# Kernel tuning notes

Measured on AMD Instinct MI355X. Metric: run time of the kernel, lower is better.

Reference implementation:

```python
import jax, jax.numpy as jnp
import numpy as np

DIM = 512
NUM_HEADS = 8
HEAD_DIM = DIM // NUM_HEADS
MAX_SIZE = 128


def setup_inputs() -> dict:
    key = jax.random.key(0)
    ks = jax.random.split(key, 13)
    B, C, H, W = 4, DIM, 128, 128
    inp = {
        "x": jax.random.normal(ks[0], (B, C, H, W), jnp.float32),
        "q_w": jax.random.normal(ks[1], (DIM, DIM), jnp.float32) * 0.02,
        "q_b": jax.random.normal(ks[2], (DIM,), jnp.float32) * 0.02,
        "k_w": jax.random.normal(ks[3], (DIM, DIM), jnp.float32) * 0.02,
        "k_b": jax.random.normal(ks[4], (DIM,), jnp.float32) * 0.02,
        "v_w": jax.random.normal(ks[5], (DIM, DIM), jnp.float32) * 0.02,
        "v_b": jax.random.normal(ks[6], (DIM,), jnp.float32) * 0.02,
        "o_w": jax.random.normal(ks[7], (DIM, DIM), jnp.float32) * 0.02,
        "o_b": jax.random.normal(ks[8], (DIM,), jnp.float32) * 0.02,
        "pos_q": jax.random.normal(ks[9], (1, NUM_HEADS, MAX_SIZE, HEAD_DIM), jnp.float32),
        "pos_k": jax.random.normal(ks[10], (1, NUM_HEADS, MAX_SIZE, HEAD_DIM), jnp.float32),
        "pos_v": jax.random.normal(ks[11], (1, NUM_HEADS, MAX_SIZE, HEAD_DIM), jnp.float32),
        "g_q": jnp.ones((1,), jnp.float32),
        "g_k": jnp.ones((1,), jnp.float32),
        "g_v1": jnp.ones((1,), jnp.float32),
        "g_v2": jnp.ones((1,), jnp.float32),
    }
    return inp


def _gated_axial_attn(x, q_w, q_b, k_w, k_b, v_w, v_b, o_w, o_b,
                      pos_q, pos_k, pos_v, g_q, g_k, g_v1, g_v2):
    B, C, H, W = x.shape
    nh, hd = NUM_HEADS, C // NUM_HEADS
    scale = hd ** (-0.5)
    # axis='width': attend along W for each (B,H) row
    xf = jnp.transpose(x, (0, 2, 3, 1)).reshape(B * H, W, C)  # (BH, W, C)

    def proj(w, b):
        y = xf @ w.T + b                       # (BH, W, C)
        return jnp.transpose(y.reshape(B * H, W, nh, hd), (0, 2, 1, 3))  # (BH, nh, W, hd)

    q = proj(q_w, q_b)
    k = proj(k_w, k_b)
    v = proj(v_w, v_b)

    pq = pos_q[0, :, :W, :]  # (nh, W, hd)
    pk = pos_k[0, :, :W, :]
    pv = pos_v[0, :, :W, :]

    # scores[i,j] = q_i.k_j + g_q * q_i.pq_j + g_k * pk_i.k_j, all scaled
    scores = jnp.einsum('bnid,bnjd->bnij', q, k)
    scores = scores + g_q[0] * jnp.einsum('bnid,njd->bnij', q, pq)
    scores = scores + g_k[0] * jnp.einsum('nid,bnjd->bnij', pk, k)
    attn = jax.nn.softmax(scores * scale, axis=-1)  # (BH, nh, W, W)

    vmix = g_v1[0] * v + g_v2[0] * pv[None]        # (BH, nh, W, hd)
    out = jnp.einsum('bnij,bnjd->bnid', attn, vmix)
    out = jnp.transpose(out, (0, 2, 1, 3)).reshape(B * H, W, C)
    out = out @ o_w.T + o_b
    return jnp.transpose(out.reshape(B, H, W, C), (0, 3, 1, 2))  # (B, C, H, W)


def reference(x, q_w, q_b, k_w, k_b, v_w, v_b, o_w, o_b,
              pos_q, pos_k, pos_v, g_q, g_k, g_v1, g_v2):
    return _gated_axial_attn(x, q_w, q_b, k_w, k_b, v_w, v_b, o_w, o_b,
                             pos_q, pos_k, pos_v, g_q, g_k, g_v1, g_v2)
```

## Files before the change

kernel.cpp:

```cpp
#include <hip/hip_runtime.h>

typedef __bf16 bf16;
typedef __attribute__((ext_vector_type(8))) __bf16 bf16x8;
typedef __attribute__((ext_vector_type(4))) __bf16 bf16x4;
typedef __attribute__((ext_vector_type(4))) float fvec4;

#define MFMA16(a, b, c) __builtin_amdgcn_mfma_f32_16x16x32_bf16(a, b, c, 0, 0, 0)

__device__ __forceinline__ void glds16(const bf16* g, bf16* l) {
  __builtin_amdgcn_global_load_lds(
      (const __attribute__((address_space(1))) void*)g,
      (__attribute__((address_space(3))) void*)l, 16, 0, 0);
}

__device__ inline fvec4 zero4() { fvec4 z = {0.f, 0.f, 0.f, 0.f}; return z; }

#define PREP_ELEMS 1245184

__global__ __launch_bounds__(512) void prep_kernel(
    const float* __restrict__ qw, const float* __restrict__ kw,
    const float* __restrict__ vw, const float* __restrict__ ow,
    const float* __restrict__ pq, const float* __restrict__ pk,
    const float* __restrict__ pv, bf16* __restrict__ dst)
{
  int i = (blockIdx.x * 512 + threadIdx.x) * 4;
  const float* s;
  if      (i < 262144)  s = qw + i;
  else if (i < 524288)  s = kw + (i - 262144);
  else if (i < 786432)  s = vw + (i - 524288);
  else if (i < 1048576) s = ow + (i - 786432);
  else if (i < 1114112) s = pq + (i - 1048576);
  else if (i < 1179648) s = pk + (i - 1114112);
  else                  s = pv + (i - 1179648);
  fvec4 v = *(const fvec4*)s;
  bf16x4 o = { (bf16)v[0], (bf16)v[1], (bf16)v[2], (bf16)v[3] };
  *(bf16x4*)(dst + i) = o;
}

__global__ __launch_bounds__(256) void xpose_kernel(
    const float* __restrict__ x, bf16* __restrict__ xt, int bh0)
{
  __shared__ float Xs[64 * 133];
  const int cb = blockIdx.x, lb = blockIdx.y;
  const int bh = bh0 + lb, b = bh >> 7, h = bh & 127;
  const int t = threadIdx.x;
  const float* xb = x + (size_t)b * 8388608 + (size_t)(cb * 64) * 16384 + h * 128;
  #pragma unroll
  for (int it = 0; it < 8; ++it) {
    int idx = it * 256 + t;
    int c = idx >> 5, w4 = (idx & 31) << 2;
    fvec4 v = *(const fvec4*)(xb + (size_t)c * 16384 + w4);
    #pragma unroll
    for (int j = 0; j < 4; ++j) Xs[c * 133 + w4 + j] = v[j];
  }
  __syncthreads();
  const int c0 = (t & 7) * 8, wsub = t >> 3;
  #pragma unroll
  for (int wb = 0; wb < 4; ++wb) {
    int w = wb * 32 + wsub;
    bf16x8 o;
    #pragma unroll
    for (int i = 0; i < 8; ++i) o[i] = (bf16)Xs[(c0 + i) * 133 + w];
    *(bf16x8*)(xt + ((size_t)lb * 128 + w) * 512 + cb * 64 + c0) = o;
  }
}

__global__ __launch_bounds__(512, 4) void qkvattn_kernel(
    const bf16* __restrict__ xt, const bf16* __restrict__ wqkv,
    const float* __restrict__ q_b, const float* __restrict__ k_b,
    const float* __restrict__ v_b, const bf16* __restrict__ posb,
    const float* __restrict__ g_q, const float* __restrict__ g_k,
    const float* __restrict__ g_v1, const float* __restrict__ g_v2,
    bf16* __restrict__ ao)
{
  __shared__ bf16 SM[26624];
  bf16* As = SM;
  bf16* Bs = SM + 8192;
  bf16* Qs = SM;
  bf16* KP = SM + 9216;
  bf16* Vt = SM;

  const int nwg = gridDim.x;
  int wg = blockIdx.x;
  wg = (wg & 7) * (nwg >> 3) + (wg >> 3);
  const int lb = wg >> 3, n = wg & 7;

  const int t = threadIdx.x;
  const int wv = t >> 6, lane = t & 63;
  const int lr = lane & 15, lg = lane >> 4;
  const int srow = lane >> 3, c16 = lane & 7;

  fvec4 acc[12];
  #pragma unroll
  for (int i = 0; i < 12; ++i) acc[i] = zero4();

  const bf16* asrc[2];
  const bf16* bsrc[3];
  #pragma unroll
  for (int j = 0; j < 2; ++j) {
    int seg = wv * 2 + j;
    int row = seg * 8 + srow;
    int cs = c16 ^ (row & 7);
    asrc[j] = xt + (size_t)(lb * 128 + row) * 512 + cs * 8;
  }
  #pragma unroll
  for (int j = 0; j < 3; ++j) {
    int seg = wv * 3 + j;
    int row = seg * 8 + srow;
    int grow = ((row >> 6) << 9) + (n << 6) + (row & 63);
    int cs = c16 ^ (row & 7);
    bsrc[j] = wqkv + (size_t)grow * 512 + cs * 8;
  }

  for (int k0 = 0; k0 < 512; k0 += 64) {
    __syncthreads();
    #pragma unroll
    for (int j = 0; j < 2; ++j)
      glds16(asrc[j] + k0, As + (wv * 2 + j) * 512);
    #pragma unroll
    for (int j = 0; j < 3; ++j)
      glds16(bsrc[j] + k0, Bs + (wv * 3 + j) * 512);
    __syncthreads();
    #pragma unroll
    for (int kc = 0; kc < 2; ++kc) {
      int arow = wv * 16 + lr;
      int acs = (kc * 4 + lg) ^ (arow & 7);
      bf16x8 af = *(const bf16x8*)(As + arow * 64 + acs * 8);
      #pragma unroll
      for (int nt = 0; nt < 12; ++nt) {
        int brow = nt * 16 + lr;
        int bcs = (kc * 4 + lg) ^ (brow & 7);
        bf16x8 bfv = *(const bf16x8*)(Bs + brow * 64 + bcs * 8);
        acc[nt] = MFMA16(af, bfv, acc[nt]);
      }
    }
  }
  __syncthreads();

  const float gq = g_q[0], gk = g_k[0], gv1 = g_v1[0], gv2 = g_v2[0];
  const bf16* pqb = posb + (size_t)n * 8192;
  const bf16* pkb = posb + 65536 + (size_t)n * 8192;
  const bf16* pvb = posb + 131072 + (size_t)n * 8192;
  const int i0 = wv * 16;

  #pragma unroll
  for (int nt = 0; nt < 4; ++nt) {
    float bq = q_b[n * 64 + nt * 16 + lr];
    #pragma unroll
    for (int r = 0; r < 4; ++r)
      Qs[(i0 + lg * 4 + r) * 72 + nt * 16 + lr] = (bf16)(acc[nt][r] + bq);
  }
  #pragma unroll
  for (int nt = 0; nt < 4; ++nt) {
    int d = nt * 16 + lr;
    float bk = k_b[n * 64 + d];
    #pragma unroll
    for (int r = 0; r < 4; ++r) {
      int jr = i0 + lg * 4 + r;
      float kv = acc[4 + nt][r] + bk;
      float pqv = (float)pqb[jr * 64 + d];
      KP[jr * 136 + d]      = (bf16)(kv + gq * pqv);
      KP[jr * 136 + 64 + d] = (bf16)kv;
    }
  }
  __syncthreads();

  fvec4 s[8];
  #pragma unroll
  for (int i = 0; i < 8; ++i) s[i] = zero4();
  #pragma unroll
  for (int kc = 0; kc < 4; ++kc) {
    bf16x8 af;
    if (kc < 2) {
      af = *(const bf16x8*)(Qs + (i0 + lr) * 72 + kc * 32 + lg * 8);
    } else {
      bf16x8 raw = *(const bf16x8*)(pkb + (i0 + lr) * 64 + (kc - 2) * 32 + lg * 8);
      #pragma unroll
      for (int i = 0; i < 8; ++i) af[i] = (bf16)(gk * (float)raw[i]);
    }
    #pragma unroll
    for (int jt = 0; jt < 8; ++jt) {
      bf16x8 bfr = *(const bf16x8*)(KP + (jt * 16 + lr) * 136 + kc * 32 + lg * 8);
      s[jt] = MFMA16(af, bfr, s[jt]);
    }
  }

  const float scale = 0.125f;
  float inv[4];
  #pragma unroll
  for (int r = 0; r < 4; ++r) {
    float m = -1e30f;
    #pragma unroll
    for (int jt = 0; jt < 8; ++jt) m = fmaxf(m, s[jt][r]);
    #pragma unroll
    for (int off = 1; off < 16; off <<= 1) m = fmaxf(m, __shfl_xor(m, off));
    float sm = 0.f;
    #pragma unroll
    for (int jt = 0; jt < 8; ++jt) {
      float e = __expf((s[jt][r] - m) * scale);
      s[jt][r] = e;
      sm += e;
    }
    #pragma unroll
    for (int off = 1; off < 16; off <<= 1) sm += __shfl_xor(sm, off);
    inv[r] = 1.f / sm;
  }
  __syncthreads();

  #pragma unroll
  for (int r = 0; r < 4; ++r) {
    int i = i0 + lg * 4 + r;
    #pragma unroll
    for (int jt = 0; jt < 8; ++jt)
      KP[i * 136 + jt * 16 + lr] = (bf16)(s[jt][r] * inv[r]);
  }
  #pragma unroll
  for (int nt = 0; nt < 4; ++nt) {
    int d = nt * 16 + lr;
    float bv = v_b[n * 64 + d];
    #pragma unroll
    for (int r = 0; r < 4; ++r) {
      int jr = i0 + lg * 4 + r;
      Vt[d * 136 + jr] =
          (bf16)(gv1 * (acc[8 + nt][r] + bv) + gv2 * (float)pvb[jr * 64 + d]);
    }
  }
  __syncthreads();

  fvec4 o[4];
  #pragma unroll
  for (int i = 0; i < 4; ++i) o[i] = zero4();
  #pragma unroll
  for (int kc = 0; kc < 4; ++kc) {
    bf16x8 af = *(const bf16x8*)(KP + (i0 + lr) * 136 + kc * 32 + lg * 8);
    #pragma unroll
    for (int dt = 0; dt < 4; ++dt) {
      bf16x8 bfr = *(const bf16x8*)(Vt + (dt * 16 + lr) * 136 + kc * 32 + lg * 8);
      o[dt] = MFMA16(af, bfr, o[dt]);
    }
  }
  #pragma unroll
  for (int dt = 0; dt < 4; ++dt) {
    #pragma unroll
    for (int r = 0; r < 4; ++r) {
      int i = i0 + lg * 4 + r;
      ao[((size_t)lb * 128 + i) * 512 + n * 64 + dt * 16 + lr] = (bf16)o[dt][r];
    }
  }
}

__global__ __launch_bounds__(256, 3) void oproj_kernel(
    const bf16* __restrict__ ao, const bf16* __restrict__ wo,
    const float* __restrict__ o_b, float* __restrict__ out, int bh0)
{
  __shared__ bf16 As[128 * 64];
  __shared__ bf16 Bs[128 * 64];
  const int nwg = gridDim.x;
  int wg = blockIdx.x;
  if ((nwg & 7) == 0) wg = (wg & 7) * (nwg >> 3) + (wg >> 3);
  const int ct4 = wg & 3;
  const int lb = wg >> 2;
  const int bh = bh0 + lb, b = bh >> 7, h = bh & 127;
  const int t = threadIdx.x;
  const int wv = t >> 6, lane = t & 63;
  const int lr = lane & 15, lg = lane >> 4;
  const int wm = wv >> 1, wn = wv & 1;
  const int srow = lane >> 3, c16 = lane & 7;

  fvec4 acc[4][4];
  #pragma unroll
  for (int i = 0; i < 4; ++i)
    #pragma unroll
    for (int j = 0; j < 4; ++j) acc[i][j] = zero4();

  for (int k0 = 0; k0 < 512; k0 += 64) {
    __syncthreads();
    #pragma unroll
    for (int j = 0; j < 4; ++j) {
      int seg = wv * 4 + j;
      int row = seg * 8 + srow;
      int cs = c16 ^ (row & 7);
      glds16(wo + (size_t)(ct4 * 128 + row) * 512 + k0 + cs * 8, As + seg * 512);
      glds16(ao + ((size_t)lb * 128 + row) * 512 + k0 + cs * 8, Bs + seg * 512);
    }
    __syncthreads();
    #pragma unroll
    for (int kc = 0; kc < 2; ++kc) {
      bf16x8 af[4], bfv[4];
      #pragma unroll
      for (int mt = 0; mt < 4; ++mt) {
        int row = wm * 64 + mt * 16 + lr;
        int cs = (kc * 4 + lg) ^ (row & 7);
        af[mt] = *(const bf16x8*)(As + row * 64 + cs * 8);
      }
      #pragma unroll
      for (int nt = 0; nt < 4; ++nt) {
        int row = wn * 64 + nt * 16 + lr;
        int cs = (kc * 4 + lg) ^ (row & 7);
        bfv[nt] = *(const bf16x8*)(Bs + row * 64 + cs * 8);
      }
      #pragma unroll
      for (int mt = 0; mt < 4; ++mt)
        #pragma unroll
        for (int nt = 0; nt < 4; ++nt)
          acc[mt][nt] = MFMA16(af[mt], bfv[nt], acc[mt][nt]);
    }
  }
  #pragma unroll
  for (int mt = 0; mt < 4; ++mt) {
    #pragma unroll
    for (int r = 0; r < 4; ++r) {
      int co = ct4 * 128 + wm * 64 + mt * 16 + lg * 4 + r;
      float bv = o_b[co];
      size_t ob = ((size_t)(b * 512 + co) * 128 + h) * 128;
      #pragma unroll
      for (int nt = 0; nt < 4; ++nt) {
        int w = wn * 64 + nt * 16 + lr;
        out[ob + w] = acc[mt][nt][r] + bv;
      }
    }
  }
}

extern "C" void kernel_launch(void* const* d_in, const int* in_sizes, int n_in,
                              void* d_out, int out_size, void* d_ws, size_t ws_size,
                              hipStream_t stream) {
  const float* x    = (const float*)d_in[0];
  const float* q_w  = (const float*)d_in[1];
  const float* q_b  = (const float*)d_in[2];
  const float* k_w  = (const float*)d_in[3];
  const float* k_b  = (const float*)d_in[4];
  const float* v_w  = (const float*)d_in[5];
  const float* v_b  = (const float*)d_in[6];
  const float* o_w  = (const float*)d_in[7];
  const float* o_b  = (const float*)d_in[8];
  const float* pos_q = (const float*)d_in[9];
  const float* pos_k = (const float*)d_in[10];
  const float* pos_v = (const float*)d_in[11];
  const float* g_q  = (const float*)d_in[12];
  const float* g_k  = (const float*)d_in[13];
  const float* g_v1 = (const float*)d_in[14];
  const float* g_v2 = (const float*)d_in[15];
  float* out = (float*)d_out;

  bf16* prep = (bf16*)d_ws;
  bf16* wqkv = prep;
  bf16* wo   = prep + 786432;
  bf16* posb = prep + 1048576;

  bf16* rest = prep + PREP_ELEMS;
  size_t avail = (ws_size > (size_t)PREP_ELEMS * 2) ? ws_size - (size_t)PREP_ELEMS * 2 : 0;
  const size_t per_bh = (size_t)(65536 + 65536) * sizeof(bf16);
  int nbh = (int)(avail / per_bh);
  if (nbh > 512) nbh = 512;
  if (nbh < 1) nbh = 1;

  bf16* xt = rest;
  bf16* ao = xt + (size_t)nbh * 65536;

  prep_kernel<<<608, 512, 0, stream>>>(q_w, k_w, v_w, o_w, pos_q, pos_k, pos_v, prep);

  for (int bh0 = 0; bh0 < 512; bh0 += nbh) {
    int cur = (512 - bh0 < nbh) ? (512 - bh0) : nbh;
    xpose_kernel<<<dim3(8, cur), 256, 0, stream>>>(x, xt, bh0);
    qkvattn_kernel<<<cur * 8, 512, 0, stream>>>(xt, wqkv, q_b, k_b, v_b, posb,
                                                g_q, g_k, g_v1, g_v2, ao);
    oproj_kernel<<<cur * 4, 256, 0, stream>>>(ao, wo, o_b, out, bh0);
  }
}
```

Before: 510.5 us.

## Double-buffer QKV GEMM loads and retile warps to 2x6 MFMA blocks

The QKV projection loop in the fused attention kernel now double-buffers its LDS tiles, prefetching the next K-slice with global_load_lds while MFMAs run on the current one, which removes one barrier per iteration. The 8 waves are rearranged into a 4x2 grid, each computing 2x6 MFMA tiles instead of 1x12, so loaded fragments are reused more. The padded LDS layouts for Q, K/P and V^T are replaced with XOR-swizzled unpadded layouts. In exchange, shared memory grows from about 52KB to 80KB per block, which may lower occupancy below the requested 4 blocks per CU, and the epilogue gains section branching.

```diff
diff --git a/kernel.cpp b/kernel.cpp
--- a/kernel.cpp
+++ b/kernel.cpp
@@ -73,11 +73,9 @@
     const float* __restrict__ g_v1, const float* __restrict__ g_v2,
     bf16* __restrict__ ao)
 {
-  __shared__ bf16 SM[26624];
-  bf16* As = SM;
-  bf16* Bs = SM + 8192;
+  __shared__ bf16 SM[40960];
   bf16* Qs = SM;
-  bf16* KP = SM + 9216;
+  bf16* KP = SM + 8192;
   bf16* Vt = SM;
 
   const int nwg = gridDim.x;
@@ -89,10 +87,13 @@
   const int wv = t >> 6, lane = t & 63;
   const int lr = lane & 15, lg = lane >> 4;
   const int srow = lane >> 3, c16 = lane & 7;
-
-  fvec4 acc[12];
-  #pragma unroll
-  for (int i = 0; i < 12; ++i) acc[i] = zero4();
+  const int wm2 = wv >> 1, wn2 = wv & 1;
+
+  fvec4 acc[2][6];
+  #pragma unroll
+  for (int i = 0; i < 2; ++i)
+    #pragma unroll
+    for (int j = 0; j < 6; ++j) acc[i][j] = zero4();
 
   const bf16* asrc[2];
   const bf16* bsrc[3];
@@ -112,28 +113,46 @@
     bsrc[j] = wqkv + (size_t)grow * 512 + cs * 8;
   }
 
+  #pragma unroll
+  for (int j = 0; j < 2; ++j) glds16(asrc[j], SM + (wv * 2 + j) * 512);
+  #pragma unroll
+  for (int j = 0; j < 3; ++j) glds16(bsrc[j], SM + 8192 + (wv * 3 + j) * 512);
+
+  int cur = 0;
   for (int k0 = 0; k0 < 512; k0 += 64) {
     __syncthreads();
-    #pragma unroll
-    for (int j = 0; j < 2; ++j)
-      glds16(asrc[j] + k0, As + (wv * 2 + j) * 512);
-    #pragma unroll
-    for (int j = 0; j < 3; ++j)
-      glds16(bsrc[j] + k0, Bs + (wv * 3 + j) * 512);
-    __syncthreads();
+    if (k0 < 448) {
+      bf16* Ad = SM + (cur ^ 1) * 20480;
+      bf16* Bd = Ad + 8192;
+      #pragma unroll
+      for (int j = 0; j < 2; ++j) glds16(asrc[j] + k0 + 64, Ad + (wv * 2 + j) * 512);
+      #pragma unroll
+      for (int j = 0; j < 3; ++j) glds16(bsrc[j] + k0 + 64, Bd + (wv * 3 + j) * 512);
+    }
+    const bf16* Ab = SM + cur * 20480;
+    const bf16* Bb = Ab + 8192;
     #pragma unroll
     for (int kc = 0; kc < 2; ++kc) {
-      int arow = wv * 16 + lr;
-      int acs = (kc * 4 + lg) ^ (arow & 7);
-      bf16x8 af = *(const bf16x8*)(As + arow * 64 + acs * 8);
-      #pragma unroll
-      for (int nt = 0; nt < 12; ++nt) {
-        int brow = nt * 16 + lr;
-        int bcs = (kc * 4 + lg) ^ (brow & 7);
-        bf16x8 bfv = *(const bf16x8*)(Bs + brow * 64 + bcs * 8);
-        acc[nt] = MFMA16(af, bfv, acc[nt]);
-      }
-    }
+      bf16x8 af[2], bfv[6];
+      #pragma unroll
+      for (int mt = 0; mt < 2; ++mt) {
+        int row = wm2 * 32 + mt * 16 + lr;
+        int cs = (kc * 4 + lg) ^ (row & 7);
+        af[mt] = *(const bf16x8*)(Ab + row * 64 + cs * 8);
+      }
+      #pragma unroll
+      for (int nt = 0; nt < 6; ++nt) {
+        int row = wn2 * 96 + nt * 16 + lr;
+        int cs = (kc * 4 + lg) ^ (row & 7);
+        bfv[nt] = *(const bf16x8*)(Bb + row * 64 + cs * 8);
+      }
+      #pragma unroll
+      for (int mt = 0; mt < 2; ++mt)
+        #pragma unroll
+        for (int nt = 0; nt < 6; ++nt)
+          acc[mt][nt] = MFMA16(af[mt], bfv[nt], acc[mt][nt]);
+    }
+    cur ^= 1;
   }
   __syncthreads();
 
@@ -141,30 +160,41 @@
   const bf16* pqb = posb + (size_t)n * 8192;
   const bf16* pkb = posb + 65536 + (size_t)n * 8192;
   const bf16* pvb = posb + 131072 + (size_t)n * 8192;
+
+  #pragma unroll
+  for (int mt = 0; mt < 2; ++mt) {
+    #pragma unroll
+    for (int nt = 0; nt < 6; ++nt) {
+      int gc = wn2 * 96 + nt * 16 + lr;
+      int sec = gc >> 6;
+      int d = gc & 63;
+      int rb = wm2 * 32 + mt * 16 + lg * 4;
+      if (sec == 0) {
+        float bq = q_b[n * 64 + d];
+        #pragma unroll
+        for (int r = 0; r < 4; ++r) {
+          int row = rb + r;
+          Qs[row * 64 + (((d >> 3) ^ (row & 7)) << 3) + (d & 7)] =
+              (bf16)(acc[mt][nt][r] + bq);
+        }
+      } else if (sec == 1) {
+        float bk = k_b[n * 64 + d];
+        #pragma unroll
+        for (int r = 0; r < 4; ++r) {
+          int row = rb + r;
+          float kv = acc[mt][nt][r] + bk;
+          float pqv = (float)pqb[row * 64 + d];
+          KP[row * 128 + (((d >> 3) ^ (row & 7)) << 3) + (d & 7)] =
+              (bf16)(kv + gq * pqv);
+          int d2 = 64 + d;
+          KP[row * 128 + (((d2 >> 3) ^ (row & 7)) << 3) + (d2 & 7)] = (bf16)kv;
+        }
+      }
+    }
+  }
+  __syncthreads();
+
   const int i0 = wv * 16;
-
-  #pragma unroll
-  for (int nt = 0; nt < 4; ++nt) {
-    float bq = q_b[n * 64 + nt * 16 + lr];
-    #pragma unroll
-    for (int r = 0; r < 4; ++r)
-      Qs[(i0 + lg * 4 + r) * 72 + nt * 16 + lr] = (bf16)(acc[nt][r] + bq);
-  }
-  #pragma unroll
-  for (int nt = 0; nt < 4; ++nt) {
-    int d = nt * 16 + lr;
-    float bk = k_b[n * 64 + d];
-    #pragma unroll
-    for (int r = 0; r < 4; ++r) {
-      int jr = i0 + lg * 4 + r;
-      float kv = acc[4 + nt][r] + bk;
-      float pqv = (float)pqb[jr * 64 + d];
-      KP[jr * 136 + d]      = (bf16)(kv + gq * pqv);
-      KP[jr * 136 + 64 + d] = (bf16)kv;
-    }
-  }
-  __syncthreads();
-
   fvec4 s[8];
   #pragma unroll
   for (int i = 0; i < 8; ++i) s[i] = zero4();
@@ -172,7 +202,9 @@
   for (int kc = 0; kc < 4; ++kc) {
     bf16x8 af;
     if (kc < 2) {
-      af = *(const bf16x8*)(Qs + (i0 + lr) * 72 + kc * 32 + lg * 8);
+      int row = i0 + lr;
+      int cs = (kc * 4 + lg) ^ (row & 7);
+      af = *(const bf16x8*)(Qs + row * 64 + cs * 8);
     } else {
       bf16x8 raw = *(const bf16x8*)(pkb + (i0 + lr) * 64 + (kc - 2) * 32 + lg * 8);
       #pragma unroll
@@ -180,7 +212,9 @@
     }
     #pragma unroll
     for (int jt = 0; jt < 8; ++jt) {
-      bf16x8 bfr = *(const bf16x8*)(KP + (jt * 16 + lr) * 136 + kc * 32 + lg * 8);
+      int row = jt * 16 + lr;
+      int cs = (kc * 4 + lg) ^ (row & 7);
+      bf16x8 bfr = *(const bf16x8*)(KP + row * 128 + cs * 8);
       s[jt] = MFMA16(af, bfr, s[jt]);
     }
   }
@@ -211,18 +245,26 @@
   for (int r = 0; r < 4; ++r) {
     int i = i0 + lg * 4 + r;
     #pragma unroll
-    for (int jt = 0; jt < 8; ++jt)
-      KP[i * 136 + jt * 16 + lr] = (bf16)(s[jt][r] * inv[r]);
-  }
-  #pragma unroll
-  for (int nt = 0; nt < 4; ++nt) {
-    int d = nt * 16 + lr;
-    float bv = v_b[n * 64 + d];
-    #pragma unroll
-    for (int r = 0; r < 4; ++r) {
-      int jr = i0 + lg * 4 + r;
-      Vt[d * 136 + jr] =
-          (bf16)(gv1 * (acc[8 + nt][r] + bv) + gv2 * (float)pvb[jr * 64 + d]);
+    for (int jt = 0; jt < 8; ++jt) {
+      int j = jt * 16 + lr;
+      KP[i * 128 + (((j >> 3) ^ (i & 7)) << 3) + (j & 7)] =
+          (bf16)(s[jt][r] * inv[r]);
+    }
+  }
+  if (wn2 == 1) {
+    #pragma unroll
+    for (int mt = 0; mt < 2; ++mt) {
+      #pragma unroll
+      for (int nt = 2; nt < 6; ++nt) {
+        int d = nt * 16 - 32 + lr;
+        float bv = v_b[n * 64 + d];
+        #pragma unroll
+        for (int r = 0; r < 4; ++r) {
+          int j = wm2 * 32 + mt * 16 + lg * 4 + r;
+          float vv = gv1 * (acc[mt][nt][r] + bv) + gv2 * (float)pvb[j * 64 + d];
+          Vt[d * 128 + (((j >> 3) ^ (d & 7)) << 3) + (j & 7)] = (bf16)vv;
+        }
+      }
     }
   }
   __syncthreads();
@@ -232,10 +274,14 @@
   for (int i = 0; i < 4; ++i) o[i] = zero4();
   #pragma unroll
   for (int kc = 0; kc < 4; ++kc) {
-    bf16x8 af = *(const bf16x8*)(KP + (i0 + lr) * 136 + kc * 32 + lg * 8);
+    int prow = i0 + lr;
+    int pcs = (kc * 4 + lg) ^ (prow & 7);
+    bf16x8 af = *(const bf16x8*)(KP + prow * 128 + pcs * 8);
     #pragma unroll
     for (int dt = 0; dt < 4; ++dt) {
-      bf16x8 bfr = *(const bf16x8*)(Vt + (dt * 16 + lr) * 136 + kc * 32 + lg * 8);
+      int vr = dt * 16 + lr;
+      int vcs = (kc * 4 + lg) ^ (vr & 7);
+      bf16x8 bfr = *(const bf16x8*)(Vt + vr * 128 + vcs * 8);
       o[dt] = MFMA16(af, bfr, o[dt]);
     }
   }
```

Measured after the change: 494.9 us. -3.1%, faster.
